# Kernel tuning notes

Hardware: AMD Instinct MI355X
Metric: run time of the kernel (lower is better)

The kernel has to match this reference:

```python
import jax, jax.numpy as jnp
import numpy as np

V = 257        # vocab size (prime -> multiplicative inverses exist mod V)
B = 64         # batch
L = 1024       # sequence length
TEMPERATURE = 1.0


def one_hot_argmax(logits, temperature):
    # hard one-hot forward, softmax-temperature backward (straight-through)
    hard = jax.nn.one_hot(jnp.argmax(logits, axis=-1), logits.shape[-1], dtype=logits.dtype)
    soft = jax.nn.softmax(logits / temperature, axis=-1)
    return soft + jax.lax.stop_gradient(hard - soft)


def setup_inputs() -> dict:
    key = jax.random.key(0)
    k1, k2, k3 = jax.random.split(key, 3)
    idx = jax.random.randint(k1, (B, L), 0, V)
    x = jax.nn.one_hot(idx, V, dtype=jnp.float32)          # [B, L, V] hard one-hot
    W = jax.random.normal(k2, (V, 2 * V), jnp.float32) * 0.05
    b = jax.random.normal(k3, (2 * V,), jnp.float32) * 0.05
    # extended-Euclid inverse table (V prime -> Fermat: a^(V-2) mod V); inv(0):=0
    inv = np.array([0] + [pow(a, V - 2, V) for a in range(1, V)], dtype=np.int32)
    return {"x": x, "W": W, "b": b, "inv_table": jnp.asarray(inv)}


def reference(x, W, b, inv_table):
    dtype = x.dtype
    u = jnp.arange(V)
    # one_hot_minus: shift_matrix[u, v] = shift[(v - u) % V]
    minus_idx = (u[None, :] - u[:, None]) % V              # [V, V]
    # one_hot_multiply: for a != 0, scaled[a, u] = inputs[(u * inv(a)) % V]
    vidx = (u[None, :] * inv_table[:, None]) % V           # [V, V]
    notzero = (u != 0).astype(dtype)[None, :, None]        # zero out scale-by-0 row

    @jax.checkpoint
    def step(prev, x_t):
        # prev: [B, V] previous output one-hot; x_t: [B, V] current input one-hot
        net = prev @ W + b                                  # [B, 2V] causal masked layer
        loc_logits, scale_logits = jnp.split(net, 2, axis=-1)
        loc = one_hot_argmax(loc_logits, TEMPERATURE)       # [B, V]
        scale = one_hot_argmax(scale_logits, TEMPERATURE)   # [B, V]
        # multiplicative inverse of scale in one-hot space (non-differentiable, as in py_func)
        inv_scale = jax.nn.one_hot(inv_table[jnp.argmax(scale, axis=-1)], V, dtype=dtype)
        # (x_t - loc) % V in one-hot space: einsum('...v,...uv->...u') with rolled loc
        shifted = jnp.einsum('bv,buv->bu', x_t, loc[:, minus_idx])
        # (shifted * inv_scale) % V in one-hot space
        scaled = shifted[:, vidx] * notzero                 # [B, V, V]
        out = jnp.einsum('ba,bau->bu', inv_scale, scaled)   # [B, V]
        return out, out

    init = jnp.zeros((x.shape[0], V), dtype)
    _, ys = jax.lax.scan(step, init, jnp.swapaxes(x, 0, 1))  # scan over L
    return jnp.swapaxes(ys, 0, 1)                            # [B, L, V]
```

## Files before the change

### kernel.cpp

```cpp
#include <hip/hip_runtime.h>
#include <stdint.h>

#define V 257
#define NB 64
#define L 1024
#define ZERO_STATE 257
#define NSTATE 258
#define CHUNKS 32
#define CLEN 32
#define EXTRACT_BLOCKS 2048
#define VECS_PER_CHUNK 2056

typedef float f32x4 __attribute__((ext_vector_type(4)));

__device__ __forceinline__ int gstep(const uint32_t* __restrict__ tbl, int p, int x) {
    uint32_t e = tbl[p];
    int ia  = (int)(e >> 16);
    int loc = (int)(e & 0xffff);
    int s = x - loc;
    s += (s >> 31) & V;
    int n = s * ia;
    int m = (n & 255) - (n >> 8);
    m += (m >> 31) & V;
    return (ia == 0) ? ZERO_STATE : m;
}

__global__ void prep(const float* __restrict__ W, const float* __restrict__ bias,
                     const int* __restrict__ inv_table, const f32x4* __restrict__ x4,
                     uint32_t* __restrict__ gtable, uint16_t* __restrict__ xidx, int n4) {
    if (blockIdx.x < NSTATE) {
        int lane = threadIdx.x;
        if (lane >= 64) return;
        int p = blockIdx.x;
        const float* wrow = (p < V) ? (W + (size_t)p * (2 * V)) : nullptr;
        float bestL = -INFINITY; int idxL = 0;
        float bestS = -INFINITY; int idxS = 0;
        for (int j = lane; j < V; j += 64) {
            float vl = wrow ? (wrow[j] + bias[j]) : bias[j];
            float vs = wrow ? (wrow[V + j] + bias[V + j]) : bias[V + j];
            if (vl > bestL) { bestL = vl; idxL = j; }
            if (vs > bestS) { bestS = vs; idxS = j; }
        }
        for (int off = 32; off >= 1; off >>= 1) {
            float oL = __shfl_down(bestL, off); int oiL = __shfl_down(idxL, off);
            float oS = __shfl_down(bestS, off); int oiS = __shfl_down(idxS, off);
            if (oL > bestL || (oL == bestL && oiL < idxL)) { bestL = oL; idxL = oiL; }
            if (oS > bestS || (oS == bestS && oiS < idxS)) { bestS = oS; idxS = oiS; }
        }
        if (lane == 0) {
            int ia = inv_table[idxS];
            gtable[p] = (uint32_t)idxL | ((uint32_t)ia << 16);
        }
        return;
    }
    int stride = EXTRACT_BLOCKS * blockDim.x;
    for (int i = (blockIdx.x - NSTATE) * blockDim.x + threadIdx.x; i < n4; i += stride) {
        f32x4 v = x4[i];
        int j = i * 4;
        if (v.x == 1.0f) { int r = j / V;       xidx[r] = (uint16_t)(j     - r * V); }
        if (v.y == 1.0f) { int r = (j + 1) / V; xidx[r] = (uint16_t)(j + 1 - r * V); }
        if (v.z == 1.0f) { int r = (j + 2) / V; xidx[r] = (uint16_t)(j + 2 - r * V); }
        if (v.w == 1.0f) { int r = (j + 3) / V; xidx[r] = (uint16_t)(j + 3 - r * V); }
    }
}

__global__ void phase1(const uint32_t* __restrict__ gtable, const uint16_t* __restrict__ xidx,
                       uint16_t* __restrict__ f) {
    __shared__ uint32_t tbl[NSTATE];
    __shared__ uint16_t xs[CLEN];
    int bc = blockIdx.x;
    int b = bc / CHUNKS, c = bc % CHUNKS;
    int tid = threadIdx.x;
    for (int j = tid; j < NSTATE; j += 128) tbl[j] = gtable[j];
    if (tid < CLEN) xs[tid] = xidx[b * L + c * CLEN + tid];
    __syncthreads();
    int p0 = tid;
    int p1 = tid + 128;
    int p2 = (tid + 256 < NSTATE) ? tid + 256 : 0;
    #pragma unroll 4
    for (int k = 0; k < CLEN; ++k) {
        int x = xs[k];
        p0 = gstep(tbl, p0, x);
        p1 = gstep(tbl, p1, x);
        p2 = gstep(tbl, p2, x);
    }
    uint16_t* frow = f + (size_t)bc * NSTATE;
    frow[tid] = (uint16_t)p0;
    frow[tid + 128] = (uint16_t)p1;
    if (tid < 2) frow[tid + 256] = (uint16_t)p2;
}

__global__ void __launch_bounds__(256)
replay_write(const uint32_t* __restrict__ gtable, const uint16_t* __restrict__ xidx,
             const uint16_t* __restrict__ f, f32x4* __restrict__ out) {
    __shared__ uint32_t tbl[NSTATE];
    __shared__ uint16_t fl[(CHUNKS - 1) * NSTATE];
    __shared__ uint16_t xs[CLEN];
    __shared__ uint16_t os[CLEN];
    int b = blockIdx.x >> 5, c = blockIdx.x & 31;
    int tid = threadIdx.x;

    for (int j = tid; j < NSTATE; j += 256) tbl[j] = gtable[j];
    int nfl = c * NSTATE;
    const uint16_t* fb = f + (size_t)b * CHUNKS * NSTATE;
    for (int j = tid; j < nfl; j += 256) fl[j] = fb[j];
    if (tid < CLEN) xs[tid] = xidx[b * L + c * CLEN + tid];
    __syncthreads();

    if (tid == 0) {
        int st = ZERO_STATE;
        for (int i = 0; i < c; ++i) st = fl[i * NSTATE + st];
        int p = st;
        for (int k = 0; k < CLEN; ++k) {
            int x = xs[k];
            uint32_t e = tbl[p];
            int ia  = (int)(e >> 16);
            int loc = (int)(e & 0xffff);
            if (ia == 0) {
                os[k] = 0xFFFF;
                p = ZERO_STATE;
            } else {
                int s = x - loc;
                s += (s >> 31) & V;
                int n = s * ia;
                int m = (n & 255) - (n >> 8);
                m += (m >> 31) & V;
                os[k] = (uint16_t)m;
                p = m;
            }
        }
    }
    __syncthreads();

    f32x4* obase = out + ((size_t)(b * L + c * CLEN) * V) / 4;
    for (int i = tid; i < VECS_PER_CHUNK; i += 256) {
        int e = i * 4;
        int r = e / V;
        int col = e - r * V;
        int h0 = os[r];
        int h1 = (col + 3 >= V) ? os[r + 1] : h0;
        f32x4 v;
        int cc = col;
        v.x = (cc == h0) ? 1.0f : 0.0f; cc++;
        if (cc == V) { cc = 0; h0 = h1; }
        v.y = (cc == h0) ? 1.0f : 0.0f; cc++;
        if (cc == V) { cc = 0; h0 = h1; }
        v.z = (cc == h0) ? 1.0f : 0.0f; cc++;
        if (cc == V) { cc = 0; h0 = h1; }
        v.w = (cc == h0) ? 1.0f : 0.0f;
        obase[i] = v;
    }
}

extern "C" void kernel_launch(void* const* d_in, const int* in_sizes, int n_in,
                              void* d_out, int out_size, void* d_ws, size_t ws_size,
                              hipStream_t stream) {
    const float* x    = (const float*)d_in[0];
    const float* W    = (const float*)d_in[1];
    const float* bias = (const float*)d_in[2];
    const int*   inv  = (const int*)d_in[3];

    uint8_t* ws = (uint8_t*)d_ws;
    uint32_t* gtable = (uint32_t*)ws;
    uint16_t* xidx   = (uint16_t*)(ws + 4096);
    uint16_t* f      = (uint16_t*)(ws + 4096 + NB * L * 2);

    int n4 = NB * L * V / 4;

    prep<<<NSTATE + EXTRACT_BLOCKS, 256, 0, stream>>>(W, bias, inv, (const f32x4*)x,
                                                      gtable, xidx, n4);
    phase1<<<NB * CHUNKS, 128, 0, stream>>>(gtable, xidx, f);
    replay_write<<<NB * CHUNKS, 256, 0, stream>>>(gtable, xidx, f, (f32x4*)d_out);
}
```

Baseline: 138.1 us.

## Fuse one-hot index extraction into chunk composition kernel, split table build

Moves the extraction of input indices from the one-hot x tensor out of the prep kernel and into the per-chunk transition-composition kernel. Each block now reads its own chunk of x, decodes indices into shared memory, composes the chunk map, and writes xidx for later use. The argmax table is built by its own small kernel. The aim is to overlap the large x read with chunk work and to avoid the extra launch-level dependency. The cost is that the table kernel now runs serially, with few blocks, before the fused kernel starts.

```diff
diff --git a/kernel.cpp b/kernel.cpp
--- a/kernel.cpp
+++ b/kernel.cpp
@@ -8,7 +8,6 @@
 #define NSTATE 258
 #define CHUNKS 32
 #define CLEN 32
-#define EXTRACT_BLOCKS 2048
 #define VECS_PER_CHUNK 2056
 
 typedef float f32x4 __attribute__((ext_vector_type(4)));
@@ -25,69 +24,64 @@
     return (ia == 0) ? ZERO_STATE : m;
 }
 
-__global__ void prep(const float* __restrict__ W, const float* __restrict__ bias,
-                     const int* __restrict__ inv_table, const f32x4* __restrict__ x4,
-                     uint32_t* __restrict__ gtable, uint16_t* __restrict__ xidx, int n4) {
-    if (blockIdx.x < NSTATE) {
-        int lane = threadIdx.x;
-        if (lane >= 64) return;
-        int p = blockIdx.x;
-        const float* wrow = (p < V) ? (W + (size_t)p * (2 * V)) : nullptr;
-        float bestL = -INFINITY; int idxL = 0;
-        float bestS = -INFINITY; int idxS = 0;
-        for (int j = lane; j < V; j += 64) {
-            float vl = wrow ? (wrow[j] + bias[j]) : bias[j];
-            float vs = wrow ? (wrow[V + j] + bias[V + j]) : bias[V + j];
-            if (vl > bestL) { bestL = vl; idxL = j; }
-            if (vs > bestS) { bestS = vs; idxS = j; }
-        }
-        for (int off = 32; off >= 1; off >>= 1) {
-            float oL = __shfl_down(bestL, off); int oiL = __shfl_down(idxL, off);
-            float oS = __shfl_down(bestS, off); int oiS = __shfl_down(idxS, off);
-            if (oL > bestL || (oL == bestL && oiL < idxL)) { bestL = oL; idxL = oiL; }
-            if (oS > bestS || (oS == bestS && oiS < idxS)) { bestS = oS; idxS = oiS; }
-        }
-        if (lane == 0) {
-            int ia = inv_table[idxS];
-            gtable[p] = (uint32_t)idxL | ((uint32_t)ia << 16);
-        }
-        return;
+__global__ void table_k(const float* __restrict__ W, const float* __restrict__ bias,
+                        const int* __restrict__ inv_table, uint32_t* __restrict__ gtable) {
+    int lane = threadIdx.x;
+    int p = blockIdx.x;
+    const float* wrow = (p < V) ? (W + (size_t)p * (2 * V)) : nullptr;
+    float bestL = -INFINITY; int idxL = 0;
+    float bestS = -INFINITY; int idxS = 0;
+    for (int j = lane; j < V; j += 64) {
+        float vl = wrow ? (wrow[j] + bias[j]) : bias[j];
+        float vs = wrow ? (wrow[V + j] + bias[V + j]) : bias[V + j];
+        if (vl > bestL) { bestL = vl; idxL = j; }
+        if (vs > bestS) { bestS = vs; idxS = j; }
     }
-    int stride = EXTRACT_BLOCKS * blockDim.x;
-    for (int i = (blockIdx.x - NSTATE) * blockDim.x + threadIdx.x; i < n4; i += stride) {
-        f32x4 v = x4[i];
-        int j = i * 4;
-        if (v.x == 1.0f) { int r = j / V;       xidx[r] = (uint16_t)(j     - r * V); }
-        if (v.y == 1.0f) { int r = (j + 1) / V; xidx[r] = (uint16_t)(j + 1 - r * V); }
-        if (v.z == 1.0f) { int r = (j + 2) / V; xidx[r] = (uint16_t)(j + 2 - r * V); }
-        if (v.w == 1.0f) { int r = (j + 3) / V; xidx[r] = (uint16_t)(j + 3 - r * V); }
+    for (int off = 32; off >= 1; off >>= 1) {
+        float oL = __shfl_down(bestL, off); int oiL = __shfl_down(idxL, off);
+        float oS = __shfl_down(bestS, off); int oiS = __shfl_down(idxS, off);
+        if (oL > bestL || (oL == bestL && oiL < idxL)) { bestL = oL; idxL = oiL; }
+        if (oS > bestS || (oS == bestS && oiS < idxS)) { bestS = oS; idxS = oiS; }
+    }
+    if (lane == 0) {
+        int ia = inv_table[idxS];
+        gtable[p] = (uint32_t)idxL | ((uint32_t)ia << 16);
     }
 }
 
-__global__ void phase1(const uint32_t* __restrict__ gtable, const uint16_t* __restrict__ xidx,
-                       uint16_t* __restrict__ f) {
+__global__ void __launch_bounds__(256)
+extract_chunks(const uint32_t* __restrict__ gtable, const f32x4* __restrict__ x4,
+               uint16_t* __restrict__ xidx, uint16_t* __restrict__ f) {
     __shared__ uint32_t tbl[NSTATE];
     __shared__ uint16_t xs[CLEN];
-    int bc = blockIdx.x;
-    int b = bc / CHUNKS, c = bc % CHUNKS;
+    int b = blockIdx.x >> 5, c = blockIdx.x & 31;
     int tid = threadIdx.x;
-    for (int j = tid; j < NSTATE; j += 128) tbl[j] = gtable[j];
-    if (tid < CLEN) xs[tid] = xidx[b * L + c * CLEN + tid];
+
+    for (int j = tid; j < NSTATE; j += 256) tbl[j] = gtable[j];
+
+    const f32x4* xbase = x4 + ((size_t)(b * L + c * CLEN) * V) / 4;
+    for (int i = tid; i < VECS_PER_CHUNK; i += 256) {
+        f32x4 v = xbase[i];
+        int e = i * 4;
+        if (v.x == 1.0f) { int r = e / V;       xs[r] = (uint16_t)(e     - r * V); }
+        if (v.y == 1.0f) { int r = (e + 1) / V; xs[r] = (uint16_t)(e + 1 - r * V); }
+        if (v.z == 1.0f) { int r = (e + 2) / V; xs[r] = (uint16_t)(e + 2 - r * V); }
+        if (v.w == 1.0f) { int r = (e + 3) / V; xs[r] = (uint16_t)(e + 3 - r * V); }
+    }
     __syncthreads();
+
     int p0 = tid;
-    int p1 = tid + 128;
-    int p2 = (tid + 256 < NSTATE) ? tid + 256 : 0;
+    int p1 = (tid < 2) ? tid + 256 : 0;
     #pragma unroll 4
     for (int k = 0; k < CLEN; ++k) {
         int x = xs[k];
         p0 = gstep(tbl, p0, x);
         p1 = gstep(tbl, p1, x);
-        p2 = gstep(tbl, p2, x);
     }
-    uint16_t* frow = f + (size_t)bc * NSTATE;
+    uint16_t* frow = f + (size_t)blockIdx.x * NSTATE;
     frow[tid] = (uint16_t)p0;
-    frow[tid + 128] = (uint16_t)p1;
-    if (tid < 2) frow[tid + 256] = (uint16_t)p2;
+    if (tid < 2) frow[tid + 256] = (uint16_t)p1;
+    if (tid < CLEN) xidx[b * L + c * CLEN + tid] = xs[tid];
 }
 
 __global__ void __launch_bounds__(256)
@@ -165,10 +159,7 @@
     uint16_t* xidx   = (uint16_t*)(ws + 4096);
     uint16_t* f      = (uint16_t*)(ws + 4096 + NB * L * 2);
 
-    int n4 = NB * L * V / 4;
-
-    prep<<<NSTATE + EXTRACT_BLOCKS, 256, 0, stream>>>(W, bias, inv, (const f32x4*)x,
-                                                      gtable, xidx, n4);
-    phase1<<<NB * CHUNKS, 128, 0, stream>>>(gtable, xidx, f);
+    table_k<<<NSTATE, 64, 0, stream>>>(W, bias, inv, gtable);
+    extract_chunks<<<NB * CHUNKS, 256, 0, stream>>>(gtable, (const f32x4*)x, xidx, f);
     replay_write<<<NB * CHUNKS, 256, 0, stream>>>(gtable, xidx, f, (f32x4*)d_out);
 }
```

New measurement: 141.7 us. +2.6%, slower.
